# Optimization experiments

Measured on AMD Instinct MI355X. Metric: run time of the kernel, lower is better.

## Reference

```python
import jax, jax.numpy as jnp
import numpy as np

K = 3          # kernel_size
STRIDE = 1
PAD = 1
DIL = 1


def conv2d(x, w, b, stride=STRIDE, pad=PAD, dil=DIL):
    y = jax.lax.conv_general_dilated(
        x, w, window_strides=(stride, stride),
        padding=((pad, pad), (pad, pad)), rhs_dilation=(dil, dil),
        dimension_numbers=('NCHW', 'OIHW', 'NCHW'))
    if b is not None:
        y = y + b[None, :, None, None]
    return y


def bilinear_gather(x, py, px):
    """Zero-padded bilinear sampling.
    x: [B,C,H,W]; py,px: [B,K2,Ho,Wo] float coords. Returns [B,C,K2,Ho,Wo].
    Matches torchvision deform_conv2d: out-of-range corners contribute zero."""
    B, C, H, W = x.shape
    y0 = jnp.floor(py)
    x0 = jnp.floor(px)
    wy1 = py - y0
    wx1 = px - x0
    wy0 = 1.0 - wy1
    wx0 = 1.0 - wx1
    xf = x.reshape(B, C, H * W)

    def corner(yi, xi, wgt):
        valid = (yi >= 0) & (yi < H) & (xi >= 0) & (xi < W)
        yc = jnp.clip(yi, 0, H - 1).astype(jnp.int32)
        xc = jnp.clip(xi, 0, W - 1).astype(jnp.int32)
        idx = (yc * W + xc).reshape(B, 1, -1)            # [B,1,K2*Ho*Wo]
        v = jnp.take_along_axis(xf, idx, axis=2)         # [B,C,K2*Ho*Wo]
        v = v.reshape(B, C, *yi.shape[1:])               # [B,C,K2,Ho,Wo]
        w = (wgt * valid.astype(x.dtype))[:, None]       # [B,1,K2,Ho,Wo]
        return v * w

    return (corner(y0, x0, wy0 * wx0) + corner(y0, x0 + 1, wy0 * wx1)
            + corner(y0 + 1, x0, wy1 * wx0) + corner(y0 + 1, x0 + 1, wy1 * wx1))


def reference(x, w_offset, b_offset, w_mask, b_mask, w_deform):
    B, C, H, W = x.shape
    K2 = K * K
    offset = conv2d(x, w_offset, b_offset)               # [B,2*K2,Ho,Wo]
    mask = jax.nn.sigmoid(conv2d(x, w_mask, b_mask))     # [B,K2,Ho,Wo]
    Ho, Wo = offset.shape[2], offset.shape[3]

    off = offset.reshape(B, K2, 2, Ho, Wo)
    dy, dx = off[:, :, 0], off[:, :, 1]                  # [B,K2,Ho,Wo]

    ky = (jnp.arange(K2) // K).astype(x.dtype) * DIL     # kernel tap row offsets
    kx = (jnp.arange(K2) % K).astype(x.dtype) * DIL
    base_y = (jnp.arange(Ho) * STRIDE - PAD).astype(x.dtype)
    base_x = (jnp.arange(Wo) * STRIDE - PAD).astype(x.dtype)
    py = dy + base_y[None, None, :, None] + ky[None, :, None, None]
    px = dx + base_x[None, None, None, :] + kx[None, :, None, None]

    val = bilinear_gather(x, py, px)                     # [B,C,K2,Ho,Wo]
    val = val * mask[:, None]                            # modulation

    w = w_deform.reshape(w_deform.shape[0], C, K2)       # [Cout,Cin,K2]
    return jnp.einsum('bckhw,ock->bohw', val, w)


def setup_inputs() -> dict:
    key = jax.random.key(0)
    k = jax.random.split(key, 6)
    B, Cin, Cout, H, W = 2, 64, 64, 224, 224
    x = jax.random.normal(k[0], (B, Cin, H, W), dtype=jnp.float32)
    # source zero-inits offset/mask convs; use small random weights to exercise
    # fractional, scattered sampling coordinates.
    w_offset = jax.random.normal(k[1], (2 * K * K, Cin, K, K), dtype=jnp.float32) * 0.01
    b_offset = jnp.zeros((2 * K * K,), dtype=jnp.float32)
    w_mask = jax.random.normal(k[2], (K * K, Cin, K, K), dtype=jnp.float32) * 0.01
    b_mask = jnp.zeros((K * K,), dtype=jnp.float32)
    w_deform = jax.random.normal(k[3], (Cout, Cin, K, K), dtype=jnp.float32) * (1.0 / np.sqrt(Cin * K * K))
    return {"x": x, "w_offset": w_offset, "b_offset": b_offset,
            "w_mask": w_mask, "b_mask": b_mask, "w_deform": w_deform}
```

## Files before the change

kernel.cpp:

```cpp
#include <hip/hip_runtime.h>
#include <hip/hip_bf16.h>
#include <math.h>

constexpr int B    = 2;
constexpr int C    = 64;
constexpr int H    = 224;
constexpr int W    = 224;
constexpr int Hp   = 226;
constexpr int Wp   = 226;
constexpr int OCO  = 18;
constexpr int OM   = 27;
constexpr int COUT = 64;
constexpr int HW   = H * W;
constexpr int NPIX = B * HW;
constexpr int CK   = C * 9;
constexpr int CPB  = 32;

constexpr int PAD_BLKS = (HW / 32) * B;
constexpr int BOR_N    = B * 900 * 8;
constexpr int BOR_BLKS = (BOR_N + 255) / 256;
constexpr int WA_BLKS  = (COUT * CK) / 256;
constexpr int WOM_BLKS = (32 * CK) / 256;

typedef short  bf16x8 __attribute__((ext_vector_type(8)));
typedef float  f32x4  __attribute__((ext_vector_type(4)));

__device__ inline unsigned short f2bf(float f) {
    union { float f; unsigned u; } v; v.f = f;
    unsigned r = v.u + 0x7FFF + ((v.u >> 16) & 1);
    return (unsigned short)(r >> 16);
}
__device__ inline unsigned cvtpk(float a, float b) {
    __hip_bfloat162 h = __float22bfloat162_rn(make_float2(a, b));
    union { __hip_bfloat162 h; unsigned u; } cv; cv.h = h;
    return cv.u;
}
__device__ inline float blo(unsigned u) { union { unsigned u; float f; } c; c.u = u << 16; return c.f; }
__device__ inline float bhi(unsigned u) { union { unsigned u; float f; } c; c.u = u & 0xFFFF0000u; return c.f; }

__global__ __launch_bounds__(256) void k_prep(const float* __restrict__ x,
                                              unsigned short* __restrict__ xp,
                                              const float* __restrict__ wd,
                                              unsigned short* __restrict__ wA,
                                              const float* __restrict__ w_off,
                                              const float* __restrict__ w_msk,
                                              const float* __restrict__ b_off,
                                              const float* __restrict__ b_msk,
                                              unsigned short* __restrict__ womA,
                                              float* __restrict__ biasv) {
    __shared__ float tile[64][33];
    const int bx  = blockIdx.x;
    const int tid = threadIdx.x;

    if (bx < PAD_BLKS) {
        const int b   = bx / (HW / 32);
        const int hw0 = (bx % (HW / 32)) * 32;
        const int hwl = tid & 31, cl = tid >> 5;
        const float* xb = x + (size_t)b * C * HW;
#pragma unroll
        for (int j = 0; j < 8; ++j) {
            int c = cl + j * 8;
            tile[c][hwl] = xb[(size_t)c * HW + hw0 + hwl];
        }
        __syncthreads();
        unsigned short* xpb = xp + (size_t)b * Hp * Wp * C;
        const int l15 = tid & 15, hh = tid >> 4;
        const int c = l15 * 4;
#pragma unroll
        for (int half = 0; half < 2; ++half) {
            int hw = hw0 + half * 16 + hh;
            int y = hw / W, xx = hw % W;
            float t0 = tile[c][half * 16 + hh],     t1 = tile[c + 1][half * 16 + hh];
            float t2 = tile[c + 2][half * 16 + hh], t3 = tile[c + 3][half * 16 + hh];
            *reinterpret_cast<uint2*>(xpb + ((size_t)(y + 1) * Wp + (xx + 1)) * C + c) =
                make_uint2(cvtpk(t0, t1), cvtpk(t2, t3));
        }
        return;
    }
    if (bx < PAD_BLKS + BOR_BLKS) {
        int i = (bx - PAD_BLKS) * 256 + tid;
        if (i >= BOR_N) return;
        int chunk = i & 7;
        int cell  = (i >> 3) % 900;
        int b     = (i >> 3) / 900;
        int y, xx;
        if      (cell < 226) { y = 0;              xx = cell; }
        else if (cell < 452) { y = Hp - 1;         xx = cell - 226; }
        else if (cell < 676) { y = cell - 452 + 1; xx = 0; }
        else                 { y = cell - 676 + 1; xx = Wp - 1; }
        uint4 z = make_uint4(0u, 0u, 0u, 0u);
        *reinterpret_cast<uint4*>(xp + ((size_t)b * Hp * Wp + y * Wp + xx) * C + chunk * 8) = z;
        return;
    }
    if (bx < PAD_BLKS + BOR_BLKS + WA_BLKS) {
        int i  = (bx - PAD_BLKS - BOR_BLKS) * 256 + tid;
        int o  = i / CK;
        int kc = i % CK;
        int k  = kc >> 6;
        int c  = kc & 63;
        wA[i] = f2bf(wd[((size_t)o * C + c) * 9 + k]);
        return;
    }
    {
        int i = (bx - PAD_BLKS - BOR_BLKS - WA_BLKS) * 256 + tid;
        if (i < 32) biasv[i] = (i < OCO) ? b_off[i] : (i < OM) ? b_msk[i - OCO] : 0.f;
        int oc = i / CK;
        int kc = i % CK;
        int k  = kc >> 6;
        int c  = kc & 63;
        float v = (oc < OCO) ? w_off[((size_t)oc * C + c) * 9 + k]
                : (oc < OM)  ? w_msk[((size_t)(oc - OCO) * C + c) * 9 + k]
                             : 0.f;
        womA[i] = f2bf(v);
    }
}

__global__ __launch_bounds__(256, 3) void k_fused(const unsigned short* __restrict__ xp,
                                                  const unsigned short* __restrict__ womA,
                                                  const unsigned short* __restrict__ wA,
                                                  const float* __restrict__ biasv,
                                                  float* __restrict__ out) {
    __shared__ __align__(16) unsigned short imcol[CPB * CK];
    __shared__ float som[CPB][28];
    __shared__ int4   gplanO[CPB * 9];
    __shared__ float4 gplanW[CPB * 9];
    const int tid  = threadIdx.x;
    const int lane = tid & 63;
    const int wv   = tid >> 6;
    const int q    = lane >> 4;
    const int l15  = lane & 15;
    int bid = blockIdx.x;
    bid = (bid & 7) * (gridDim.x >> 3) + (bid >> 3);
    const int pix0 = bid * CPB;
    const int bb   = pix0 / HW;
    const unsigned short* xb = xp + (size_t)bb * Hp * Wp * C;

    const int c0 = l15 * 4;

    {
        uint2 va[2][9];
#pragma unroll
        for (int pi = 0; pi < 2; ++pi) {
            const int p_local = pi * 16 + wv * 4 + q;
            const int pix = pix0 + p_local;
            const int hw  = pix - bb * HW;
            const int y   = hw / W;
            const int xx  = hw % W;
#pragma unroll
            for (int k = 0; k < 9; ++k) {
                const int ky = k / 3, kx = k % 3;
                va[pi][k] = *reinterpret_cast<const uint2*>(
                    xb + ((size_t)(y + ky) * Wp + (xx + kx)) * C + c0);
            }
        }
#pragma unroll
        for (int pi = 0; pi < 2; ++pi) {
            const int p_local = pi * 16 + wv * 4 + q;
            int wbase = p_local * (CK * 2) + l15 * 8;
            wbase ^= (p_local & 7) << 4;
#pragma unroll
            for (int k = 0; k < 9; ++k)
                *reinterpret_cast<uint2*>(reinterpret_cast<char*>(imcol) + wbase + k * 128) = va[pi][k];
        }
    }
    __syncthreads();

    {
        f32x4 acc = {0.f, 0.f, 0.f, 0.f};
        const int m = wv & 1, n = wv >> 1;
        const unsigned short* a0 = womA + (size_t)(m * 16 + l15) * CK;
        const int row = n * 16 + l15;
#pragma unroll 3
        for (int ks = 0; ks < 18; ++ks) {
            int byte = row * (CK * 2) + ks * 64 + q * 16;
            byte ^= (row & 7) << 4;
            const bf16x8 bfv = *reinterpret_cast<const bf16x8*>(
                reinterpret_cast<const char*>(imcol) + byte);
            const bf16x8 af = *reinterpret_cast<const bf16x8*>(a0 + ks * 32 + q * 8);
            acc = __builtin_amdgcn_mfma_f32_16x16x32_bf16(af, bfv, acc, 0, 0, 0);
        }
        const int pp = n * 16 + l15;
#pragma unroll
        for (int r = 0; r < 4; ++r) {
            const int oc = m * 16 + q * 4 + r;
            if (oc < OM) {
                float v = acc[r] + biasv[oc];
                som[pp][oc] = (oc < OCO) ? v : 1.0f / (1.0f + __expf(-v));
            }
        }
    }
    __syncthreads();

    for (int e = tid; e < CPB * 9; e += 256) {
        const int pe = e / 9;
        const int k  = e - pe * 9;
        const int pix = pix0 + pe;
        const int hw  = pix - bb * HW;
        const int ho  = hw / W;
        const int wo  = hw - ho * W;
        const int ky  = k / 3, kx = k - (k / 3) * 3;
        const float dy = som[pe][2 * k];
        const float dx = som[pe][2 * k + 1];
        const float mm = som[pe][OCO + k];
        const float py = dy + (float)(ho + ky - 1);
        const float px = dx + (float)(wo + kx - 1);
        const float fy = floorf(py), fx = floorf(px);
        const int   y0 = (int)fy,   x0 = (int)fx;
        const float wy1 = py - fy,  wx1 = px - fx;
        const float wy0 = 1.f - wy1, wx0 = 1.f - wx1;
        const bool iy0 = (y0 >= 0) & (y0 < H);
        const bool iy1 = (y0 + 1 >= 0) & (y0 + 1 < H);
        const bool ix0 = (x0 >= 0) & (x0 < W);
        const bool ix1 = (x0 + 1 >= 0) & (x0 + 1 < W);
        const int ya = min(max(y0 + 1, 0), Hp - 1);
        const int yb = min(max(y0 + 2, 0), Hp - 1);
        const int xa = min(max(x0 + 1, 0), Wp - 1);
        const int xc = min(max(x0 + 2, 0), Wp - 1);
        const int rA = ya * Wp, rB = yb * Wp;
        gplanO[e] = make_int4((rA + xa) * C, (rA + xc) * C,
                              (rB + xa) * C, (rB + xc) * C);
        gplanW[e] = make_float4(
            wy0 * wx0 * mm * ((iy0 & ix0) ? 1.f : 0.f),
            wy0 * wx1 * mm * ((iy0 & ix1) ? 1.f : 0.f),
            wy1 * wx0 * mm * ((iy1 & ix0) ? 1.f : 0.f),
            wy1 * wx1 * mm * ((iy1 & ix1) ? 1.f : 0.f));
    }
    __syncthreads();

#pragma unroll
    for (int pi = 0; pi < 2; ++pi) {
        const int p_local = pi * 16 + wv * 4 + q;
        int wbase = p_local * (CK * 2) + l15 * 8;
        wbase ^= (p_local & 7) << 4;
        int4   po[9];
        float4 pw[9];
#pragma unroll
        for (int k = 0; k < 9; ++k) {
            po[k] = gplanO[p_local * 9 + k];
            pw[k] = gplanW[p_local * 9 + k];
        }
        uint2 u00[9], u01[9], u10[9], u11[9];
#pragma unroll
        for (int k = 0; k < 9; ++k) {
            u00[k] = *reinterpret_cast<const uint2*>(xb + po[k].x + c0);
            u01[k] = *reinterpret_cast<const uint2*>(xb + po[k].y + c0);
            u10[k] = *reinterpret_cast<const uint2*>(xb + po[k].z + c0);
            u11[k] = *reinterpret_cast<const uint2*>(xb + po[k].w + c0);
        }
#pragma unroll
        for (int k = 0; k < 9; ++k) {
            const float4 wt = pw[k];
            const float s0 = wt.x * blo(u00[k].x) + wt.y * blo(u01[k].x) + wt.z * blo(u10[k].x) + wt.w * blo(u11[k].x);
            const float s1 = wt.x * bhi(u00[k].x) + wt.y * bhi(u01[k].x) + wt.z * bhi(u10[k].x) + wt.w * bhi(u11[k].x);
            const float s2 = wt.x * blo(u00[k].y) + wt.y * blo(u01[k].y) + wt.z * blo(u10[k].y) + wt.w * blo(u11[k].y);
            const float s3 = wt.x * bhi(u00[k].y) + wt.y * bhi(u01[k].y) + wt.z * bhi(u10[k].y) + wt.w * bhi(u11[k].y);
            *reinterpret_cast<uint2*>(reinterpret_cast<char*>(imcol) + wbase + k * 128) =
                make_uint2(cvtpk(s0, s1), cvtpk(s2, s3));
        }
    }
    __syncthreads();

    f32x4 acc[2] = {{0.f,0.f,0.f,0.f},{0.f,0.f,0.f,0.f}};
    const unsigned short* wrow = wA + (size_t)(wv * 16 + l15) * CK;
#pragma unroll 3
    for (int ks = 0; ks < 18; ++ks) {
        const bf16x8 af = *reinterpret_cast<const bf16x8*>(wrow + ks * 32 + q * 8);
#pragma unroll
        for (int nt = 0; nt < 2; ++nt) {
            const int row = nt * 16 + l15;
            int byte = row * (CK * 2) + ks * 64 + q * 16;
            byte ^= (row & 7) << 4;
            const bf16x8 bfv = *reinterpret_cast<const bf16x8*>(
                reinterpret_cast<const char*>(imcol) + byte);
            acc[nt] = __builtin_amdgcn_mfma_f32_16x16x32_bf16(af, bfv, acc[nt], 0, 0, 0);
        }
    }

    const int o0 = wv * 16 + q * 4;
#pragma unroll
    for (int nt = 0; nt < 2; ++nt) {
        const int pixn = pix0 + nt * 16 + l15;
        const int hw   = pixn - bb * HW;
#pragma unroll
        for (int r = 0; r < 4; ++r)
            out[((size_t)bb * COUT + o0 + r) * HW + hw] = acc[nt][r];
    }
}

extern "C" void kernel_launch(void* const* d_in, const int* in_sizes, int n_in,
                              void* d_out, int out_size, void* d_ws, size_t ws_size,
                              hipStream_t stream) {
    const float* x     = (const float*)d_in[0];
    const float* w_off = (const float*)d_in[1];
    const float* b_off = (const float*)d_in[2];
    const float* w_msk = (const float*)d_in[3];
    const float* b_msk = (const float*)d_in[4];
    const float* w_def = (const float*)d_in[5];
    float* out = (float*)d_out;

    unsigned short* xpadT = (unsigned short*)d_ws;
    float* biasv = (float*)(xpadT + (size_t)B * Hp * Wp * C);
    unsigned short* wA   = (unsigned short*)(biasv + 32);
    unsigned short* womA = wA + (size_t)COUT * CK;

    k_prep<<<PAD_BLKS + BOR_BLKS + WA_BLKS + WOM_BLKS, 256, 0, stream>>>(
        x, xpadT, w_def, wA, w_off, w_msk, b_off, b_msk, womA, biasv);
    k_fused<<<NPIX / CPB, 256, 0, stream>>>(xpadT, womA, wA, biasv, out);
}
```

Measured before the change: 177.1 us.

## Compute bilinear plan per-lane, drop LDS plan buffers, raise occupancy

Removes the shared-memory gather-plan arrays and the barrier around them. Each lane now recomputes the sampling offsets and weights for its own pixel and taps straight from the offset/mask values in shared memory. The kernel's occupancy hint goes from 3 to 4 blocks per SM, and the im2col staging no longer holds all loads in registers before storing. The prep kernel also loads x with float4 vector reads. This cuts LDS use and a sync, but each of the 16 lanes sharing a pixel repeats the coordinate math, and the tighter register budget may cause spills.

```diff
diff --git a/kernel.cpp b/kernel.cpp
--- a/kernel.cpp
+++ b/kernel.cpp
@@ -55,12 +55,17 @@
     if (bx < PAD_BLKS) {
         const int b   = bx / (HW / 32);
         const int hw0 = (bx % (HW / 32)) * 32;
-        const int hwl = tid & 31, cl = tid >> 5;
         const float* xb = x + (size_t)b * C * HW;
-#pragma unroll
-        for (int j = 0; j < 8; ++j) {
-            int c = cl + j * 8;
-            tile[c][hwl] = xb[(size_t)c * HW + hw0 + hwl];
+        {
+            const int c  = tid >> 2;
+            const int hq = (tid & 3) * 8;
+            const float* src = xb + (size_t)c * HW + hw0 + hq;
+            const float4 a0 = *reinterpret_cast<const float4*>(src);
+            const float4 a1 = *reinterpret_cast<const float4*>(src + 4);
+            tile[c][hq + 0] = a0.x; tile[c][hq + 1] = a0.y;
+            tile[c][hq + 2] = a0.z; tile[c][hq + 3] = a0.w;
+            tile[c][hq + 4] = a1.x; tile[c][hq + 5] = a1.y;
+            tile[c][hq + 6] = a1.z; tile[c][hq + 7] = a1.w;
         }
         __syncthreads();
         unsigned short* xpb = xp + (size_t)b * Hp * Wp * C;
@@ -115,15 +120,13 @@
     }
 }
 
-__global__ __launch_bounds__(256, 3) void k_fused(const unsigned short* __restrict__ xp,
+__global__ __launch_bounds__(256, 4) void k_fused(const unsigned short* __restrict__ xp,
                                                   const unsigned short* __restrict__ womA,
                                                   const unsigned short* __restrict__ wA,
                                                   const float* __restrict__ biasv,
                                                   float* __restrict__ out) {
     __shared__ __align__(16) unsigned short imcol[CPB * CK];
     __shared__ float som[CPB][28];
-    __shared__ int4   gplanO[CPB * 9];
-    __shared__ float4 gplanW[CPB * 9];
     const int tid  = threadIdx.x;
     const int lane = tid & 63;
     const int wv   = tid >> 6;
@@ -137,30 +140,21 @@
 
     const int c0 = l15 * 4;
 
-    {
-        uint2 va[2][9];
-#pragma unroll
-        for (int pi = 0; pi < 2; ++pi) {
-            const int p_local = pi * 16 + wv * 4 + q;
-            const int pix = pix0 + p_local;
-            const int hw  = pix - bb * HW;
-            const int y   = hw / W;
-            const int xx  = hw % W;
-#pragma unroll
-            for (int k = 0; k < 9; ++k) {
-                const int ky = k / 3, kx = k % 3;
-                va[pi][k] = *reinterpret_cast<const uint2*>(
-                    xb + ((size_t)(y + ky) * Wp + (xx + kx)) * C + c0);
-            }
-        }
-#pragma unroll
-        for (int pi = 0; pi < 2; ++pi) {
-            const int p_local = pi * 16 + wv * 4 + q;
-            int wbase = p_local * (CK * 2) + l15 * 8;
-            wbase ^= (p_local & 7) << 4;
-#pragma unroll
-            for (int k = 0; k < 9; ++k)
-                *reinterpret_cast<uint2*>(reinterpret_cast<char*>(imcol) + wbase + k * 128) = va[pi][k];
+#pragma unroll
+    for (int pi = 0; pi < 2; ++pi) {
+        const int p_local = pi * 16 + wv * 4 + q;
+        const int pix = pix0 + p_local;
+        const int hw  = pix - bb * HW;
+        const int y   = hw / W;
+        const int xx  = hw % W;
+        int wbase = p_local * (CK * 2) + l15 * 8;
+        wbase ^= (p_local & 7) << 4;
+#pragma unroll
+        for (int k = 0; k < 9; ++k) {
+            const int ky = k / 3, kx = k % 3;
+            const uint2 v = *reinterpret_cast<const uint2*>(
+                xb + ((size_t)(y + ky) * Wp + (xx + kx)) * C + c0);
+            *reinterpret_cast<uint2*>(reinterpret_cast<char*>(imcol) + wbase + k * 128) = v;
         }
     }
     __syncthreads();
@@ -191,54 +185,48 @@
     }
     __syncthreads();
 
-    for (int e = tid; e < CPB * 9; e += 256) {
-        const int pe = e / 9;
-        const int k  = e - pe * 9;
-        const int pix = pix0 + pe;
+#pragma unroll
+    for (int pi = 0; pi < 2; ++pi) {
+        const int p_local = pi * 16 + wv * 4 + q;
+        const int pix = pix0 + p_local;
         const int hw  = pix - bb * HW;
         const int ho  = hw / W;
         const int wo  = hw - ho * W;
-        const int ky  = k / 3, kx = k - (k / 3) * 3;
-        const float dy = som[pe][2 * k];
-        const float dx = som[pe][2 * k + 1];
-        const float mm = som[pe][OCO + k];
-        const float py = dy + (float)(ho + ky - 1);
-        const float px = dx + (float)(wo + kx - 1);
-        const float fy = floorf(py), fx = floorf(px);
-        const int   y0 = (int)fy,   x0 = (int)fx;
-        const float wy1 = py - fy,  wx1 = px - fx;
-        const float wy0 = 1.f - wy1, wx0 = 1.f - wx1;
-        const bool iy0 = (y0 >= 0) & (y0 < H);
-        const bool iy1 = (y0 + 1 >= 0) & (y0 + 1 < H);
-        const bool ix0 = (x0 >= 0) & (x0 < W);
-        const bool ix1 = (x0 + 1 >= 0) & (x0 + 1 < W);
-        const int ya = min(max(y0 + 1, 0), Hp - 1);
-        const int yb = min(max(y0 + 2, 0), Hp - 1);
-        const int xa = min(max(x0 + 1, 0), Wp - 1);
-        const int xc = min(max(x0 + 2, 0), Wp - 1);
-        const int rA = ya * Wp, rB = yb * Wp;
-        gplanO[e] = make_int4((rA + xa) * C, (rA + xc) * C,
-                              (rB + xa) * C, (rB + xc) * C);
-        gplanW[e] = make_float4(
-            wy0 * wx0 * mm * ((iy0 & ix0) ? 1.f : 0.f),
-            wy0 * wx1 * mm * ((iy0 & ix1) ? 1.f : 0.f),
-            wy1 * wx0 * mm * ((iy1 & ix0) ? 1.f : 0.f),
-            wy1 * wx1 * mm * ((iy1 & ix1) ? 1.f : 0.f));
-    }
-    __syncthreads();
-
-#pragma unroll
-    for (int pi = 0; pi < 2; ++pi) {
-        const int p_local = pi * 16 + wv * 4 + q;
         int wbase = p_local * (CK * 2) + l15 * 8;
         wbase ^= (p_local & 7) << 4;
+
         int4   po[9];
         float4 pw[9];
 #pragma unroll
         for (int k = 0; k < 9; ++k) {
-            po[k] = gplanO[p_local * 9 + k];
-            pw[k] = gplanW[p_local * 9 + k];
-        }
+            const int ky = k / 3, kx = k - (k / 3) * 3;
+            const float dy = som[p_local][2 * k];
+            const float dx = som[p_local][2 * k + 1];
+            const float mm = som[p_local][OCO + k];
+            const float py = dy + (float)(ho + ky - 1);
+            const float px = dx + (float)(wo + kx - 1);
+            const float fy = floorf(py), fx = floorf(px);
+            const int   y0 = (int)fy,   x0 = (int)fx;
+            const float wy1 = py - fy,  wx1 = px - fx;
+            const float wy0 = 1.f - wy1, wx0 = 1.f - wx1;
+            const bool iy0 = (y0 >= 0) & (y0 < H);
+            const bool iy1 = (y0 + 1 >= 0) & (y0 + 1 < H);
+            const bool ix0 = (x0 >= 0) & (x0 < W);
+            const bool ix1 = (x0 + 1 >= 0) & (x0 + 1 < W);
+            const int ya = min(max(y0 + 1, 0), Hp - 1);
+            const int yb = min(max(y0 + 2, 0), Hp - 1);
+            const int xa = min(max(x0 + 1, 0), Wp - 1);
+            const int xc = min(max(x0 + 2, 0), Wp - 1);
+            const int rA = ya * Wp, rB = yb * Wp;
+            po[k] = make_int4((rA + xa) * C, (rA + xc) * C,
+                              (rB + xa) * C, (rB + xc) * C);
+            pw[k] = make_float4(
+                wy0 * wx0 * mm * ((iy0 & ix0) ? 1.f : 0.f),
+                wy0 * wx1 * mm * ((iy0 & ix1) ? 1.f : 0.f),
+                wy1 * wx0 * mm * ((iy1 & ix0) ? 1.f : 0.f),
+                wy1 * wx1 * mm * ((iy1 & ix1) ? 1.f : 0.f));
+        }
+
         uint2 u00[9], u01[9], u10[9], u11[9];
 #pragma unroll
         for (int k = 0; k < 9; ++k) {
```

Result: slower. 186.5 us (+5.3%).
